# Performance work log

Hardware: AMD Instinct MI355X
Metric: run time of the kernel (lower is better)

## Reference

```python
import jax, jax.numpy as jnp
import numpy as np

B, D, HID, DC, K = 32768, 64, 512, 128, 12
CLAMP = 1.0
L1 = D // 2          # GLOW split lengths
L2 = D - L1
INIT = 0.01          # torch code rescales all params to 0.01*randn


def setup_inputs() -> dict:
    key = jax.random.key(0)
    ks = iter(jax.random.split(key, 16))
    # FrEIA PermuteRandom: np.random.seed(k); np.random.permutation(D)
    perms = jnp.asarray(
        np.stack([np.random.RandomState(k).permutation(D) for k in range(K)]),
        dtype=jnp.int32)
    f32 = jnp.float32
    return {
        'q_feat': jax.random.normal(next(ks), (B, 1, D), f32),
        'H': jax.random.normal(next(ks), (B, DC), f32),
        'perms': perms,
        'an_logscale': INIT * jax.random.normal(next(ks), (K, D), f32),
        'an_bias': INIT * jax.random.normal(next(ks), (K, D), f32),
        's1_W1': INIT * jax.random.normal(next(ks), (K, HID, L1 + DC), f32),
        's1_b1': INIT * jax.random.normal(next(ks), (K, HID), f32),
        's1_W2': INIT * jax.random.normal(next(ks), (K, 2 * L2, HID), f32),
        's1_b2': INIT * jax.random.normal(next(ks), (K, 2 * L2), f32),
        's2_W1': INIT * jax.random.normal(next(ks), (K, HID, L2 + DC), f32),
        's2_b1': INIT * jax.random.normal(next(ks), (K, HID), f32),
        's2_W2': INIT * jax.random.normal(next(ks), (K, 2 * L1, HID), f32),
        's2_b2': INIT * jax.random.normal(next(ks), (K, 2 * L1), f32),
    }


def _mlp(x, W1, b1, W2, b2):
    # torch Linear: y = x @ W.T + b
    h = jax.nn.relu(x @ W1.T + b1)
    return h @ W2.T + b2


def _log_e(s):
    # FrEIA GLOW soft clamp: log e(s) = clamp * 0.636 * atan(s / clamp)
    return CLAMP * 0.636 * jnp.arctan(s / CLAMP)


def reference(q_feat, H, perms, an_logscale, an_bias,
              s1_W1, s1_b1, s1_W2, s1_b2,
              s2_W1, s2_b1, s2_W2, s2_b2):
    x = q_feat.reshape(q_feat.shape[0], -1)          # Flatten: (B,1,D)->(B,D)
    logj = jnp.zeros(x.shape[0], x.dtype)

    def block(carry, p):
        x, logj = carry
        perm, ls, bi, w11, b11, w12, b12, w21, b21, w22, b22 = p
        x = x[:, perm]                               # PermuteRandom (logdet 0)
        x = x * jnp.exp(ls) + bi                     # ActNorm
        logj = logj + jnp.sum(ls)
        x1, x2 = x[:, :L1], x[:, L1:]                # GLOW coupling
        r2 = _mlp(jnp.concatenate([x2, H], 1), w21, b21, w22, b22)
        le2 = _log_e(r2[:, :L1])
        y1 = jnp.exp(le2) * x1 + r2[:, L1:]
        r1 = _mlp(jnp.concatenate([y1, H], 1), w11, b11, w12, b12)
        le1 = _log_e(r1[:, :L2])
        y2 = jnp.exp(le1) * x2 + r1[:, L2:]
        logj = logj + jnp.sum(le1, axis=1) + jnp.sum(le2, axis=1)
        return (jnp.concatenate([y1, y2], 1), logj), None

    (z, logj), _ = jax.lax.scan(
        block, (x, logj),
        (perms, an_logscale, an_bias,
         s1_W1, s1_b1, s1_W2, s1_b2,
         s2_W1, s2_b1, s2_W2, s2_b2))
    return z, logj
```

## Files before the change

kernel.cpp:

```cpp
#include <hip/hip_runtime.h>
#include <hip/hip_bf16.h>
#include <math.h>

#define B_ROWS 32768

typedef __attribute__((ext_vector_type(8)))  short        s8v;
typedef __attribute__((ext_vector_type(4)))  float        f4v;
typedef __attribute__((ext_vector_type(2)))  unsigned int u2v;
typedef __attribute__((ext_vector_type(4)))  unsigned int u4v;

__device__ __forceinline__ short f2bf(float f){
  unsigned u = __builtin_bit_cast(unsigned, f);
  u = (u + 0x7fffu + ((u >> 16) & 1u)) >> 16;
  return (short)u;
}
__device__ __forceinline__ unsigned cpk(float a, float b){
  __hip_bfloat16_raw lo = (__hip_bfloat16_raw)__float2bfloat16(a);
  __hip_bfloat16_raw hi = (__hip_bfloat16_raw)__float2bfloat16(b);
  return (unsigned)lo.x | ((unsigned)hi.x << 16);
}
__device__ __forceinline__ float bf_lo(unsigned u){ return __builtin_bit_cast(float, u << 16); }
__device__ __forceinline__ float bf_hi(unsigned u){ return __builtin_bit_cast(float, u & 0xffff0000u); }

#define MFMA16(A,B,C) __builtin_amdgcn_mfma_f32_16x16x32_bf16((A),(B),(C),0,0,0)

typedef __attribute__((address_space(1))) const unsigned int gu32;
typedef __attribute__((address_space(3))) unsigned int lu32;
__device__ __forceinline__ void gl_lds16(const unsigned short* g, char* l){
  __builtin_amdgcn_global_load_lds((gu32*)(const void*)g, (lu32*)(void*)l, 16, 0, 0);
}

#define OXFT 0
#define XFT_S 132
#define OHB   33792
#define HB_S  136
#define OW1   68608
#define W1BUF 40960
#define OLJ   150528
#define OPERM 151040
#define OELS  151296
#define OBIV  151552
#define OSLS  151808
#define SM_SZ 151812

#define SL_S 68
#define SLOT_B 17408
#define OSLB1 (OW1 + W1BUF)

#define WF_W2 1966080
#define W_TOTAL 2752512

__global__ void cvtw_frag(const float* __restrict__ s1w1, const float* __restrict__ s1w2,
                          const float* __restrict__ s2w1, const float* __restrict__ s2w2,
                          unsigned short* __restrict__ dst)
{
  long t = (long)blockIdx.x * blockDim.x + threadIdx.x;
  if (t >= W_TOTAL) return;
  float v;
  if (t < WF_W2){
    int m = (int)(t / 81920); int r = (int)(t - (long)m*81920);
    int c = r / 20480;  int r2 = r - c*20480;
    int tile = r2 >> 9; int r3 = r2 & 511;
    int lane = r3 >> 3; int e = r3 & 7;
    int rg = tile / 5,  kk = tile - rg*5;
    int l15 = lane & 15, lq = lane >> 4;
    int h  = c*128 + rg*16 + l15;
    int ki = kk*32 + lq*8 + e;
    const float* src = (m & 1) ? s1w1 : s2w1;
    v = src[(size_t)(m >> 1)*81920 + h*160 + ki];
  } else {
    long u = t - WF_W2;
    int m = (int)(u / 32768); int r = (int)(u - (long)m*32768);
    int g = r >> 9; int r3 = r & 511;
    int lane = r3 >> 3; int e = r3 & 7;
    int c = g >> 4, hw = (g >> 2) & 3, ot = g & 3;
    int l15 = lane & 15, lq = lane >> 4;
    int o = ot*16 + l15;
    int h = c*128 + hw*32 + lq*8 + e;
    const float* src = (m & 1) ? s1w2 : s2w2;
    v = src[(size_t)(m >> 1)*32768 + o*512 + h];
  }
  dst[t] = (unsigned short)f2bf(v);
}

__global__ __launch_bounds__(512, 1) void cinn_dma(
    const float* __restrict__ q, const float* __restrict__ Hg,
    const int* __restrict__ perms,
    const float* __restrict__ ls_g, const float* __restrict__ bi_g,
    const float* __restrict__ s1b1, const float* __restrict__ s1b2,
    const float* __restrict__ s2b1, const float* __restrict__ s2b2,
    const unsigned short* __restrict__ wbf,
    float* __restrict__ outz, float* __restrict__ outlj)
{
  __shared__ __align__(16) char sm[SM_SZ];
  const int tid = threadIdx.x;
  const int rowbase = blockIdx.x * 128;
  const int lane = tid & 63, wave = tid >> 6;
  const int hw = wave >> 1, ng = wave & 1;
  const int l15 = lane & 15, lq = lane >> 4;

  float* XFT = (float*)(sm + OXFT);
  short* HB  = (short*)(sm + OHB);
  float* LOGJ= (float*)(sm + OLJ);
  int*   PERM= (int*)(sm + OPERM);
  float* ELS = (float*)(sm + OELS);
  float* BIV = (float*)(sm + OBIV);
  float* SLSp= (float*)(sm + OSLS);

  {
    int b = tid >> 2, j = tid & 3;
    const float* src = q + (size_t)(rowbase + b)*64 + j*16;
    #pragma unroll
    for (int i = 0; i < 4; ++i){
      f4v v = *(const f4v*)(src + 4*i);
      #pragma unroll
      for (int jj = 0; jj < 4; ++jj)
        XFT[(j*16 + 4*i + jj)*XFT_S + b] = v[jj];
    }
  }
  if (tid < 128) LOGJ[tid] = 0.f;
  if (tid == 0)  *SLSp = 0.f;
  __syncthreads();
  if (tid < 64){
    float p = 0.f;
    #pragma unroll
    for (int k = 0; k < 12; ++k) p += ls_g[k*64 + tid];
    atomicAdd(SLSp, p);
  }

  s8v hfr[4][4];
  #pragma unroll
  for (int nt = 0; nt < 4; ++nt){
    int b = rowbase + ng*64 + nt*16 + l15;
    #pragma unroll
    for (int kkh = 0; kkh < 4; ++kkh){
      const float* hp = Hg + (size_t)b*128 + kkh*32 + lq*8;
      f4v a = *(const f4v*)hp;
      f4v c = *(const f4v*)(hp + 4);
      u4v u = {cpk(a[0],a[1]), cpk(a[2],a[3]), cpk(c[0],c[1]), cpk(c[2],c[3])};
      hfr[nt][kkh] = __builtin_bit_cast(s8v, u);
    }
  }

  {
    const unsigned short* g = wbf + wave*2560 + lane*8;
    char* lb = sm + OW1 + wave*5120;
    #pragma unroll
    for (int k = 0; k < 5; ++k) gl_lds16(g + k*512, lb + k*1024);
  }

  for (int m = 0; m < 24; ++m){
    const int bp = m & 1;
    const unsigned short* w1sec = wbf + (size_t)m*81920;
    const unsigned short* w2sec = wbf + WF_W2 + (size_t)m*32768;
    const float* b1p = ((bp ? s1b1 : s2b1) + (m >> 1)*512);
    const float* b2p = ((bp ? s1b2 : s2b2) + (m >> 1)*64);

    if (!bp){
      int blk = m >> 1;
      if (tid < 64){
        PERM[tid] = perms[blk*64 + tid];
        ELS[tid]  = __expf(ls_g[blk*64 + tid]);
        BIV[tid]  = bi_g[blk*64 + tid];
      }
      __syncthreads();
      {
        int d = lane, bg = wave;
        int pd = PERM[d];
        f4v v[4];
        #pragma unroll
        for (int i = 0; i < 4; ++i)
          v[i] = *(const f4v*)(XFT + pd*XFT_S + bg*16 + 4*i);
        __syncthreads();
        float e = ELS[d], bi = BIV[d];
        #pragma unroll
        for (int i = 0; i < 4; ++i){
          #pragma unroll
          for (int jj = 0; jj < 4; ++jj) v[i][jj] = fmaf(v[i][jj], e, bi);
          *(f4v*)(XFT + d*XFT_S + bg*16 + 4*i) = v[i];
        }
      }
      __syncthreads();
    }

    const int xbase = bp ? 0 : 32;
    s8v xk[4];
    #pragma unroll
    for (int nt = 0; nt < 4; ++nt){
      int b = ng*64 + nt*16 + l15;
      const float* xp = XFT + (xbase + lq*8)*XFT_S + b;
      u4v u;
      #pragma unroll
      for (int p = 0; p < 4; ++p)
        u[p] = cpk(xp[(2*p)*XFT_S], xp[(2*p+1)*XFT_S]);
      xk[nt] = __builtin_bit_cast(s8v, u);
    }

    f4v b2v[4];
    if (hw == 0){
      #pragma unroll
      for (int ot = 0; ot < 4; ++ot)
        b2v[ot] = *(const f4v*)(b2p + ot*16 + lq*4);
    }

    f4v racc[4][4];
    #pragma unroll
    for (int ot = 0; ot < 4; ++ot)
      #pragma unroll
      for (int nt = 0; nt < 4; ++nt)
        racc[ot][nt] = (f4v){0.f,0.f,0.f,0.f};

    #pragma unroll
    for (int c = 0; c < 4; ++c){
      if (!(m == 23 && c == 3)){
        const unsigned short* gsec = (c < 3) ? w1sec : (w1sec + 81920);
        const int cn = (c < 3) ? c + 1 : 0;
        const unsigned short* g = gsec + cn*20480 + wave*2560 + lane*8;
        char* lb = sm + OW1 + ((c+1)&1)*W1BUF + wave*5120;
        #pragma unroll
        for (int k = 0; k < 5; ++k) gl_lds16(g + k*512, lb + k*1024);
      }
      s8v w2c[4];
      #pragma unroll
      for (int ot = 0; ot < 4; ++ot)
        w2c[ot] = *(const s8v*)(w2sec + ((c*4 + hw)*4 + ot)*512 + lane*8);
      f4v b1v0 = *(const f4v*)(b1p + c*128 + hw*32 + lq*4);
      f4v b1v1 = *(const f4v*)(b1p + c*128 + hw*32 + 16 + lq*4);

      const short* W1c = (const short*)(sm + OW1 + (c&1)*W1BUF);
      f4v acc[2][4];
      #pragma unroll
      for (int mt = 0; mt < 2; ++mt)
        #pragma unroll
        for (int nt = 0; nt < 4; ++nt) acc[mt][nt] = (f4v){0.f,0.f,0.f,0.f};
      #pragma unroll
      for (int kk = 0; kk < 5; ++kk){
        s8v a0 = *(const s8v*)(W1c + ((hw*2 + 0)*5 + kk)*512 + lane*8);
        s8v a1 = *(const s8v*)(W1c + ((hw*2 + 1)*5 + kk)*512 + lane*8);
        #pragma unroll
        for (int nt = 0; nt < 4; ++nt){
          s8v bb = (kk == 0) ? xk[nt] : hfr[nt][kk-1];
          acc[0][nt] = MFMA16(a0, bb, acc[0][nt]);
          acc[1][nt] = MFMA16(a1, bb, acc[1][nt]);
        }
      }
      #pragma unroll
      for (int mt = 0; mt < 2; ++mt){
        f4v bv = mt ? b1v1 : b1v0;
        #pragma unroll
        for (int nt = 0; nt < 4; ++nt){
          float h0 = fmaxf(acc[mt][nt][0] + bv[0], 0.f);
          float h1 = fmaxf(acc[mt][nt][1] + bv[1], 0.f);
          float h2 = fmaxf(acc[mt][nt][2] + bv[2], 0.f);
          float h3 = fmaxf(acc[mt][nt][3] + bv[3], 0.f);
          *(u2v*)(HB + (ng*64 + nt*16 + l15)*HB_S + hw*32 + mt*16 + lq*4) = (u2v){cpk(h0,h1), cpk(h2,h3)};
        }
      }
      #pragma unroll
      for (int nt = 0; nt < 4; ++nt){
        s8v bb = *(const s8v*)(HB + (ng*64 + nt*16 + l15)*HB_S + hw*32 + lq*8);
        #pragma unroll
        for (int ot = 0; ot < 4; ++ot)
          racc[ot][nt] = MFMA16(w2c[ot], bb, racc[ot][nt]);
      }
      __syncthreads();
    }

    {
      short* SL = (hw < 2) ? (short*)(sm + OSLB1 + hw*SLOT_B)
                           : (short*)(sm + OHB + (hw-2)*SLOT_B);
      #pragma unroll
      for (int ot = 0; ot < 4; ++ot)
        #pragma unroll
        for (int nt = 0; nt < 4; ++nt){
          float r0 = racc[ot][nt][0], r1 = racc[ot][nt][1];
          float r2 = racc[ot][nt][2], r3 = racc[ot][nt][3];
          if (hw == 0){ r0 += b2v[ot][0]; r1 += b2v[ot][1]; r2 += b2v[ot][2]; r3 += b2v[ot][3]; }
          *(u2v*)(SL + (ng*64 + nt*16 + l15)*SL_S + ot*16 + lq*4) = (u2v){cpk(r0,r1), cpk(r2,r3)};
        }
    }
    __syncthreads();

    {
      int b = tid & 127, og = tid >> 7;
      float le[8] = {0,0,0,0,0,0,0,0}, ra[8] = {0,0,0,0,0,0,0,0};
      #pragma unroll
      for (int ms = 0; ms < 4; ++ms){
        const short* SL = (ms < 2) ? (const short*)(sm + OSLB1 + ms*SLOT_B)
                                   : (const short*)(sm + OHB + (ms-2)*SLOT_B);
        u2v L0 = *(const u2v*)(SL + b*SL_S + og*8);
        u2v L1 = *(const u2v*)(SL + b*SL_S + og*8 + 4);
        u2v R0 = *(const u2v*)(SL + b*SL_S + 32 + og*8);
        u2v R1 = *(const u2v*)(SL + b*SL_S + 32 + og*8 + 4);
        le[0]+=bf_lo(L0[0]); le[1]+=bf_hi(L0[0]); le[2]+=bf_lo(L0[1]); le[3]+=bf_hi(L0[1]);
        le[4]+=bf_lo(L1[0]); le[5]+=bf_hi(L1[0]); le[6]+=bf_lo(L1[1]); le[7]+=bf_hi(L1[1]);
        ra[0]+=bf_lo(R0[0]); ra[1]+=bf_hi(R0[0]); ra[2]+=bf_lo(R0[1]); ra[3]+=bf_hi(R0[1]);
        ra[4]+=bf_lo(R1[0]); ra[5]+=bf_hi(R1[0]); ra[6]+=bf_lo(R1[1]); ra[7]+=bf_hi(R1[1]);
      }
      float part = 0.f;
      #pragma unroll
      for (int j = 0; j < 8; ++j){
        float l = 0.636f * atanf(le[j]);
        int d = bp*32 + og*8 + j;
        float y = __expf(l) * XFT[d*XFT_S + b] + ra[j];
        XFT[d*XFT_S + b] = y;
        part += l;
      }
      atomicAdd(&LOGJ[b], part);
    }
    __syncthreads();
  }

  {
    int b = tid >> 2, j = tid & 3;
    float* dst = outz + (size_t)(rowbase + b)*64 + j*16;
    #pragma unroll
    for (int i = 0; i < 4; ++i){
      f4v w;
      #pragma unroll
      for (int jj = 0; jj < 4; ++jj)
        w[jj] = XFT[(j*16 + 4*i + jj)*XFT_S + b];
      *(f4v*)(dst + 4*i) = w;
    }
  }
  if (tid < 128) outlj[rowbase + tid] = LOGJ[tid] + *SLSp;
}

extern "C" void kernel_launch(void* const* d_in, const int* in_sizes, int n_in,
                              void* d_out, int out_size, void* d_ws, size_t ws_size,
                              hipStream_t stream)
{
  const float* q    = (const float*)d_in[0];
  const float* Hg   = (const float*)d_in[1];
  const int*   perms= (const int*)  d_in[2];
  const float* ls   = (const float*)d_in[3];
  const float* bi   = (const float*)d_in[4];
  const float* s1W1 = (const float*)d_in[5];
  const float* s1b1 = (const float*)d_in[6];
  const float* s1W2 = (const float*)d_in[7];
  const float* s1b2 = (const float*)d_in[8];
  const float* s2W1 = (const float*)d_in[9];
  const float* s2b1 = (const float*)d_in[10];
  const float* s2W2 = (const float*)d_in[11];
  const float* s2b2 = (const float*)d_in[12];
  float* outz  = (float*)d_out;
  float* outlj = outz + (size_t)B_ROWS * 64;

  unsigned short* wbf = (unsigned short*)d_ws;
  cvtw_frag<<<2688, 1024, 0, stream>>>(s1W1, s1W2, s2W1, s2W2, wbf);
  cinn_dma<<<256, 512, 0, stream>>>(q, Hg, perms, ls, bi,
                                    s1b1, s1b2, s2b1, s2b2,
                                    wbf, outz, outlj);
}
```

Before: 262.3 us.

## Halve row tile to 64, run two blocks per CU with single W1 buffer

The fused flow kernel now processes 64 rows per 256-thread block, and two blocks are expected to share a CU (launch bounds 256,2) in place of one 512-thread block with 128 rows. Shared memory is cut to about 80KB by dropping the W1 double buffer. The next W1 chunk is loaded only after the first GEMM, so that load overlaps the second GEMM instead, and each wave now computes 64 hidden rows. A bf16 copy of the x-half (XHB) is kept so MFMA operands load directly, and the permutation/actnorm parameters are read straight into registers. The trade is more total weight traffic (each block streams all weights for half the rows) and less prefetch slack, in exchange for two independent blocks hiding each other's barriers and latency.

```diff
diff --git a/kernel.cpp b/kernel.cpp
--- a/kernel.cpp
+++ b/kernel.cpp
@@ -31,21 +31,16 @@
 }
 
 #define OXFT 0
-#define XFT_S 132
-#define OHB   33792
-#define HB_S  136
-#define OW1   68608
-#define W1BUF 40960
-#define OLJ   150528
-#define OPERM 151040
-#define OELS  151296
-#define OBIV  151552
-#define OSLS  151808
-#define SM_SZ 151812
-
+#define XFT_S 68
+#define OXHB 17408
+#define XHB_S 40
+#define OHB  22528
+#define HB_S 136
 #define SL_S 68
-#define SLOT_B 17408
-#define OSLB1 (OW1 + W1BUF)
+#define SLOT_B 8704
+#define OW1  39936
+#define OLJ  80896
+#define SM_SZ 81152
 
 #define WF_W2 1966080
 #define W_TOTAL 2752512
@@ -73,17 +68,17 @@
     int m = (int)(u / 32768); int r = (int)(u - (long)m*32768);
     int g = r >> 9; int r3 = r & 511;
     int lane = r3 >> 3; int e = r3 & 7;
-    int c = g >> 4, hw = (g >> 2) & 3, ot = g & 3;
+    int c = g >> 4, hs = (g >> 2) & 3, ot = g & 3;
     int l15 = lane & 15, lq = lane >> 4;
     int o = ot*16 + l15;
-    int h = c*128 + hw*32 + lq*8 + e;
+    int h = c*128 + hs*32 + lq*8 + e;
     const float* src = (m & 1) ? s1w2 : s2w2;
     v = src[(size_t)(m >> 1)*32768 + o*512 + h];
   }
   dst[t] = (unsigned short)f2bf(v);
 }
 
-__global__ __launch_bounds__(512, 1) void cinn_dma(
+__global__ __launch_bounds__(256, 2) void cinn_dma(
     const float* __restrict__ q, const float* __restrict__ Hg,
     const int* __restrict__ perms,
     const float* __restrict__ ls_g, const float* __restrict__ bi_g,
@@ -94,18 +89,15 @@
 {
   __shared__ __align__(16) char sm[SM_SZ];
   const int tid = threadIdx.x;
-  const int rowbase = blockIdx.x * 128;
+  const int rowbase = blockIdx.x * 64;
   const int lane = tid & 63, wave = tid >> 6;
   const int hw = wave >> 1, ng = wave & 1;
   const int l15 = lane & 15, lq = lane >> 4;
 
   float* XFT = (float*)(sm + OXFT);
+  short* XHB = (short*)(sm + OXHB);
   short* HB  = (short*)(sm + OHB);
   float* LOGJ= (float*)(sm + OLJ);
-  int*   PERM= (int*)(sm + OPERM);
-  float* ELS = (float*)(sm + OELS);
-  float* BIV = (float*)(sm + OBIV);
-  float* SLSp= (float*)(sm + OSLS);
 
   {
     int b = tid >> 2, j = tid & 3;
@@ -118,20 +110,13 @@
         XFT[(j*16 + 4*i + jj)*XFT_S + b] = v[jj];
     }
   }
-  if (tid < 128) LOGJ[tid] = 0.f;
-  if (tid == 0)  *SLSp = 0.f;
+  if (tid < 64) LOGJ[tid] = 0.f;
   __syncthreads();
-  if (tid < 64){
-    float p = 0.f;
-    #pragma unroll
-    for (int k = 0; k < 12; ++k) p += ls_g[k*64 + tid];
-    atomicAdd(SLSp, p);
-  }
-
-  s8v hfr[4][4];
+
+  s8v hfr[2][4];
   #pragma unroll
-  for (int nt = 0; nt < 4; ++nt){
-    int b = rowbase + ng*64 + nt*16 + l15;
+  for (int nt = 0; nt < 2; ++nt){
+    int b = rowbase + ng*32 + nt*16 + l15;
     #pragma unroll
     for (int kkh = 0; kkh < 4; ++kkh){
       const float* hp = Hg + (size_t)b*128 + kkh*32 + lq*8;
@@ -143,58 +128,50 @@
   }
 
   {
-    const unsigned short* g = wbf + wave*2560 + lane*8;
-    char* lb = sm + OW1 + wave*5120;
-    #pragma unroll
-    for (int k = 0; k < 5; ++k) gl_lds16(g + k*512, lb + k*1024);
+    const unsigned short* g = wbf + wave*5120 + lane*8;
+    char* lb = sm + OW1 + wave*10240;
+    #pragma unroll
+    for (int k = 0; k < 10; ++k) gl_lds16(g + k*512, lb + k*1024);
   }
 
   for (int m = 0; m < 24; ++m){
     const int bp = m & 1;
     const unsigned short* w1sec = wbf + (size_t)m*81920;
     const unsigned short* w2sec = wbf + WF_W2 + (size_t)m*32768;
-    const float* b1p = ((bp ? s1b1 : s2b1) + (m >> 1)*512);
-    const float* b2p = ((bp ? s1b2 : s2b2) + (m >> 1)*64);
+    const float* b1p = (bp ? s1b1 : s2b1) + (m >> 1)*512;
+    const float* b2p = (bp ? s1b2 : s2b2) + (m >> 1)*64;
 
     if (!bp){
       int blk = m >> 1;
-      if (tid < 64){
-        PERM[tid] = perms[blk*64 + tid];
-        ELS[tid]  = __expf(ls_g[blk*64 + tid]);
-        BIV[tid]  = bi_g[blk*64 + tid];
-      }
+      int   pd = perms[blk*64 + lane];
+      float e  = __expf(ls_g[blk*64 + lane]);
+      float bi = bi_g[blk*64 + lane];
+      int bg = wave;
+      f4v v[4];
+      #pragma unroll
+      for (int i = 0; i < 4; ++i)
+        v[i] = *(const f4v*)(XFT + pd*XFT_S + bg*16 + 4*i);
       __syncthreads();
-      {
-        int d = lane, bg = wave;
-        int pd = PERM[d];
-        f4v v[4];
+      #pragma unroll
+      for (int i = 0; i < 4; ++i){
+        #pragma unroll
+        for (int jj = 0; jj < 4; ++jj) v[i][jj] = fmaf(v[i][jj], e, bi);
+        *(f4v*)(XFT + lane*XFT_S + bg*16 + 4*i) = v[i];
+      }
+      if (lane >= 32){
         #pragma unroll
         for (int i = 0; i < 4; ++i)
-          v[i] = *(const f4v*)(XFT + pd*XFT_S + bg*16 + 4*i);
-        __syncthreads();
-        float e = ELS[d], bi = BIV[d];
-        #pragma unroll
-        for (int i = 0; i < 4; ++i){
           #pragma unroll
-          for (int jj = 0; jj < 4; ++jj) v[i][jj] = fmaf(v[i][jj], e, bi);
-          *(f4v*)(XFT + d*XFT_S + bg*16 + 4*i) = v[i];
-        }
+          for (int jj = 0; jj < 4; ++jj)
+            XHB[(bg*16 + 4*i + jj)*XHB_S + (lane - 32)] = f2bf(v[i][jj]);
       }
       __syncthreads();
     }
 
-    const int xbase = bp ? 0 : 32;
-    s8v xk[4];
-    #pragma unroll
-    for (int nt = 0; nt < 4; ++nt){
-      int b = ng*64 + nt*16 + l15;
-      const float* xp = XFT + (xbase + lq*8)*XFT_S + b;
-      u4v u;
-      #pragma unroll
-      for (int p = 0; p < 4; ++p)
-        u[p] = cpk(xp[(2*p)*XFT_S], xp[(2*p+1)*XFT_S]);
-      xk[nt] = __builtin_bit_cast(s8v, u);
-    }
+    s8v xk[2];
+    #pragma unroll
+    for (int nt = 0; nt < 2; ++nt)
+      xk[nt] = *(const s8v*)(XHB + (ng*32 + nt*16 + l15)*XHB_S + lq*8);
 
     f4v b2v[4];
     if (hw == 0){
@@ -203,91 +180,102 @@
         b2v[ot] = *(const f4v*)(b2p + ot*16 + lq*4);
     }
 
-    f4v racc[4][4];
+    f4v racc[4][2];
     #pragma unroll
     for (int ot = 0; ot < 4; ++ot)
       #pragma unroll
-      for (int nt = 0; nt < 4; ++nt)
+      for (int nt = 0; nt < 2; ++nt)
         racc[ot][nt] = (f4v){0.f,0.f,0.f,0.f};
 
     #pragma unroll
     for (int c = 0; c < 4; ++c){
-      if (!(m == 23 && c == 3)){
-        const unsigned short* gsec = (c < 3) ? w1sec : (w1sec + 81920);
-        const int cn = (c < 3) ? c + 1 : 0;
-        const unsigned short* g = gsec + cn*20480 + wave*2560 + lane*8;
-        char* lb = sm + OW1 + ((c+1)&1)*W1BUF + wave*5120;
-        #pragma unroll
-        for (int k = 0; k < 5; ++k) gl_lds16(g + k*512, lb + k*1024);
-      }
-      s8v w2c[4];
-      #pragma unroll
-      for (int ot = 0; ot < 4; ++ot)
-        w2c[ot] = *(const s8v*)(w2sec + ((c*4 + hw)*4 + ot)*512 + lane*8);
-      f4v b1v0 = *(const f4v*)(b1p + c*128 + hw*32 + lq*4);
-      f4v b1v1 = *(const f4v*)(b1p + c*128 + hw*32 + 16 + lq*4);
-
-      const short* W1c = (const short*)(sm + OW1 + (c&1)*W1BUF);
-      f4v acc[2][4];
-      #pragma unroll
-      for (int mt = 0; mt < 2; ++mt)
-        #pragma unroll
-        for (int nt = 0; nt < 4; ++nt) acc[mt][nt] = (f4v){0.f,0.f,0.f,0.f};
+      s8v w2c[2][4];
+      #pragma unroll
+      for (int kk2 = 0; kk2 < 2; ++kk2)
+        #pragma unroll
+        for (int ot = 0; ot < 4; ++ot)
+          w2c[kk2][ot] = *(const s8v*)(w2sec + (size_t)((c*4 + hw*2 + kk2)*4 + ot)*512 + lane*8);
+      f4v b1v[4];
+      #pragma unroll
+      for (int mt = 0; mt < 4; ++mt)
+        b1v[mt] = *(const f4v*)(b1p + c*128 + hw*64 + mt*16 + lq*4);
+
+      const short* W1c = (const short*)(sm + OW1);
+      f4v acc[4][2];
+      #pragma unroll
+      for (int mt = 0; mt < 4; ++mt)
+        #pragma unroll
+        for (int nt = 0; nt < 2; ++nt) acc[mt][nt] = (f4v){0.f,0.f,0.f,0.f};
       #pragma unroll
       for (int kk = 0; kk < 5; ++kk){
-        s8v a0 = *(const s8v*)(W1c + ((hw*2 + 0)*5 + kk)*512 + lane*8);
-        s8v a1 = *(const s8v*)(W1c + ((hw*2 + 1)*5 + kk)*512 + lane*8);
-        #pragma unroll
-        for (int nt = 0; nt < 4; ++nt){
+        s8v a[4];
+        #pragma unroll
+        for (int mt = 0; mt < 4; ++mt)
+          a[mt] = *(const s8v*)(W1c + ((hw*4 + mt)*5 + kk)*512 + lane*8);
+        #pragma unroll
+        for (int nt = 0; nt < 2; ++nt){
           s8v bb = (kk == 0) ? xk[nt] : hfr[nt][kk-1];
-          acc[0][nt] = MFMA16(a0, bb, acc[0][nt]);
-          acc[1][nt] = MFMA16(a1, bb, acc[1][nt]);
+          #pragma unroll
+          for (int mt = 0; mt < 4; ++mt)
+            acc[mt][nt] = MFMA16(a[mt], bb, acc[mt][nt]);
         }
       }
       #pragma unroll
-      for (int mt = 0; mt < 2; ++mt){
-        f4v bv = mt ? b1v1 : b1v0;
-        #pragma unroll
-        for (int nt = 0; nt < 4; ++nt){
+      for (int mt = 0; mt < 4; ++mt){
+        f4v bv = b1v[mt];
+        #pragma unroll
+        for (int nt = 0; nt < 2; ++nt){
           float h0 = fmaxf(acc[mt][nt][0] + bv[0], 0.f);
           float h1 = fmaxf(acc[mt][nt][1] + bv[1], 0.f);
           float h2 = fmaxf(acc[mt][nt][2] + bv[2], 0.f);
           float h3 = fmaxf(acc[mt][nt][3] + bv[3], 0.f);
-          *(u2v*)(HB + (ng*64 + nt*16 + l15)*HB_S + hw*32 + mt*16 + lq*4) = (u2v){cpk(h0,h1), cpk(h2,h3)};
+          *(u2v*)(HB + (ng*32 + nt*16 + l15)*HB_S + hw*64 + mt*16 + lq*4) = (u2v){cpk(h0,h1), cpk(h2,h3)};
         }
       }
-      #pragma unroll
-      for (int nt = 0; nt < 4; ++nt){
-        s8v bb = *(const s8v*)(HB + (ng*64 + nt*16 + l15)*HB_S + hw*32 + lq*8);
-        #pragma unroll
-        for (int ot = 0; ot < 4; ++ot)
-          racc[ot][nt] = MFMA16(w2c[ot], bb, racc[ot][nt]);
-      }
       __syncthreads();
+
+      if (!(m == 23 && c == 3)){
+        const unsigned short* gsec = (c < 3) ? w1sec : (w1sec + 81920);
+        const int cn = (c < 3) ? c + 1 : 0;
+        const unsigned short* g = gsec + cn*20480 + wave*5120 + lane*8;
+        char* lb = sm + OW1 + wave*10240;
+        #pragma unroll
+        for (int k = 0; k < 10; ++k) gl_lds16(g + k*512, lb + k*1024);
+      }
+
+      #pragma unroll
+      for (int kk2 = 0; kk2 < 2; ++kk2){
+        #pragma unroll
+        for (int nt = 0; nt < 2; ++nt){
+          s8v bb = *(const s8v*)(HB + (ng*32 + nt*16 + l15)*HB_S + hw*64 + kk2*32 + lq*8);
+          #pragma unroll
+          for (int ot = 0; ot < 4; ++ot)
+            racc[ot][nt] = MFMA16(w2c[kk2][ot], bb, racc[ot][nt]);
+        }
+      }
+      __syncthreads();
     }
 
     {
-      short* SL = (hw < 2) ? (short*)(sm + OSLB1 + hw*SLOT_B)
-                           : (short*)(sm + OHB + (hw-2)*SLOT_B);
+      short* SL = (short*)(sm + OHB + hw*SLOT_B);
       #pragma unroll
       for (int ot = 0; ot < 4; ++ot)
         #pragma unroll
-        for (int nt = 0; nt < 4; ++nt){
+        for (int nt = 0; nt < 2; ++nt){
           float r0 = racc[ot][nt][0], r1 = racc[ot][nt][1];
           float r2 = racc[ot][nt][2], r3 = racc[ot][nt][3];
           if (hw == 0){ r0 += b2v[ot][0]; r1 += b2v[ot][1]; r2 += b2v[ot][2]; r3 += b2v[ot][3]; }
-          *(u2v*)(SL + (ng*64 + nt*16 + l15)*SL_S + ot*16 + lq*4) = (u2v){cpk(r0,r1), cpk(r2,r3)};
+          *(u2v*)(SL + (ng*32 + nt*16 + l15)*SL_S + ot*16 + lq*4) = (u2v){cpk(r0,r1), cpk(r2,r3)};
         }
     }
     __syncthreads();
 
     {
-      int b = tid & 127, og = tid >> 7;
+      int b = tid & 63, og = tid >> 6;
       float le[8] = {0,0,0,0,0,0,0,0}, ra[8] = {0,0,0,0,0,0,0,0};
       #pragma unroll
-      for (int ms = 0; ms < 4; ++ms){
-        const short* SL = (ms < 2) ? (const short*)(sm + OSLB1 + ms*SLOT_B)
-                                   : (const short*)(sm + OHB + (ms-2)*SLOT_B);
+      for (int ms = 0; ms < 2; ++ms){
+        const short* SL = (const short*)(sm + OHB + ms*SLOT_B);
         u2v L0 = *(const u2v*)(SL + b*SL_S + og*8);
         u2v L1 = *(const u2v*)(SL + b*SL_S + og*8 + 4);
         u2v R0 = *(const u2v*)(SL + b*SL_S + 32 + og*8);
@@ -297,14 +285,18 @@
         ra[0]+=bf_lo(R0[0]); ra[1]+=bf_hi(R0[0]); ra[2]+=bf_lo(R0[1]); ra[3]+=bf_hi(R0[1]);
         ra[4]+=bf_lo(R1[0]); ra[5]+=bf_hi(R1[0]); ra[6]+=bf_lo(R1[1]); ra[7]+=bf_hi(R1[1]);
       }
-      float part = 0.f;
+      float part = 0.f, y[8];
       #pragma unroll
       for (int j = 0; j < 8; ++j){
         float l = 0.636f * atanf(le[j]);
         int d = bp*32 + og*8 + j;
-        float y = __expf(l) * XFT[d*XFT_S + b] + ra[j];
-        XFT[d*XFT_S + b] = y;
+        y[j] = __expf(l) * XFT[d*XFT_S + b] + ra[j];
+        XFT[d*XFT_S + b] = y[j];
         part += l;
+      }
+      if (!bp){
+        u4v u = {cpk(y[0],y[1]), cpk(y[2],y[3]), cpk(y[4],y[5]), cpk(y[6],y[7])};
+        *(u4v*)(XHB + b*XHB_S + og*8) = u;
       }
       atomicAdd(&LOGJ[b], part);
     }
@@ -323,7 +315,14 @@
       *(f4v*)(dst + 4*i) = w;
     }
   }
-  if (tid < 128) outlj[rowbase + tid] = LOGJ[tid] + *SLSp;
+  if (tid < 64){
+    float p = 0.f;
+    #pragma unroll
+    for (int k = 0; k < 12; ++k) p += ls_g[k*64 + tid];
+    #pragma unroll
+    for (int off = 1; off < 64; off <<= 1) p += __shfl_xor(p, off);
+    outlj[rowbase + tid] = LOGJ[tid] + p;
+  }
 }
 
 extern "C" void kernel_launch(void* const* d_in, const int* in_sizes, int n_in,
@@ -348,7 +347,7 @@
 
   unsigned short* wbf = (unsigned short*)d_ws;
   cvtw_frag<<<2688, 1024, 0, stream>>>(s1W1, s1W2, s2W1, s2W2, wbf);
-  cinn_dma<<<256, 512, 0, stream>>>(q, Hg, perms, ls, bi,
+  cinn_dma<<<512, 256, 0, stream>>>(q, Hg, perms, ls, bi,
                                     s1b1, s1b2, s2b1, s2b2,
                                     wbf, outz, outlj);
 }
```

Result: slower. 272.5 us (+3.9%).
